# Kernel tuning notes

Hardware: AMD Instinct MI355X
Metric: run time of the kernel (lower is better)

The kernel has to match this reference:

```python
import jax, jax.numpy as jnp
import numpy as np

D = 512  # feature_dim


def _attn(q, k, v, Wq, bq, Wk, bk, Wv, bv):
    # Linear uses y = x @ W.T + b (torch convention)
    Q = jnp.einsum('bnd,od->bno', q, Wq) + bq
    K = jnp.einsum('bnd,od->bno', k, Wk) + bk
    V = jnp.einsum('bnd,od->bno', v, Wv) + bv
    scale = 1.0 / jnp.sqrt(jnp.asarray(Q.shape[-1], Q.dtype))
    scores = jnp.einsum('bqo,bko->bqk', Q, K) * scale
    attn = jax.nn.softmax(scores, axis=-1)
    return jnp.einsum('bqk,bko->bqo', attn, V)


def setup_inputs() -> dict:
    key = jax.random.key(0)
    ks = jax.random.split(key, 9)
    B, N = 8, 2048
    Itime = jax.random.normal(ks[0], (B, N, D), jnp.float32)
    Ispace = jax.random.normal(ks[1], (B, N, D), jnp.float32)
    x_origin = jax.random.normal(ks[2], (B, N, N), jnp.float32)
    # stacked params for the 4 attention blocks:
    # 0: temporal_self, 1: spatial_self, 2: temporal_guides_spatial, 3: spatial_guides_temporal
    Wq = jax.random.normal(ks[3], (4, D, D), jnp.float32) * 0.02
    Wk = jax.random.normal(ks[4], (4, D, D), jnp.float32) * 0.02
    Wv = jax.random.normal(ks[5], (4, D, D), jnp.float32) * 0.02
    bq = jax.random.normal(ks[6], (4, D), jnp.float32) * 0.02
    bk = jax.random.normal(ks[7], (4, D), jnp.float32) * 0.02
    bv = jax.random.normal(ks[8], (4, D), jnp.float32) * 0.02
    return {"Itime": Itime, "Ispace": Ispace, "x_origin": x_origin,
            "Wq": Wq, "bq": bq, "Wk": Wk, "bk": bk, "Wv": Wv, "bv": bv}


def reference(Itime, Ispace, x_origin, Wq, bq, Wk, bk, Wv, bv):
    FTT = _attn(Itime, Itime, Itime, Wq[0], bq[0], Wk[0], bk[0], Wv[0], bv[0])
    FSS = _attn(Ispace, Ispace, Ispace, Wq[1], bq[1], Wk[1], bk[1], Wv[1], bv[1])
    FTS = _attn(Itime, Ispace, Ispace, Wq[2], bq[2], Wk[2], bk[2], Wv[2], bv[2])
    FST = _attn(Ispace, Itime, Itime, Wq[3], bq[3], Wk[3], bk[3], Wv[3], bv[3])
    B, N = x_origin.shape[0], x_origin.shape[1]
    res = x_origin.reshape(B, N, -1)
    return jnp.einsum('bno,bmo->bnm', FTT + FTS, FSS + FST) + res
```

## Files before the change

### kernel.cpp

```cpp
#include <hip/hip_runtime.h>
#include <stdint.h>

typedef __bf16 bf16_t;
typedef bf16_t bf16x8 __attribute__((ext_vector_type(8)));
typedef float floatx4 __attribute__((ext_vector_type(4)));
typedef ushort ushortx8 __attribute__((ext_vector_type(8)));

__device__ __forceinline__ ushort f2bf(float f) {
  uint u = __float_as_uint(f);
  u += 0x7FFFu + ((u >> 16) & 1u);
  return (ushort)(u >> 16);
}
__device__ __forceinline__ float bf2f(ushort h) {
  return __uint_as_float(((uint)h) << 16);
}

__device__ __forceinline__ void async_cp16(const ushort* g, ushort* l) {
  __builtin_amdgcn_global_load_lds(
      (const __attribute__((address_space(1))) uint32_t*)g,
      (__attribute__((address_space(3))) uint32_t*)l, 16, 0, 0);
}

__global__ __launch_bounds__(256) void cvt_f32_bf16(const float* __restrict__ in,
                                                    ushort* __restrict__ out,
                                                    long long n) {
  long long i = (((long long)blockIdx.x) * 256 + threadIdx.x) * 4;
  if (i + 3 < n) {
    float4 f = *(const float4*)(in + i);
    ushort4 o = make_ushort4(f2bf(f.x), f2bf(f.y), f2bf(f.z), f2bf(f.w));
    *(ushort4*)(out + i) = o;
  }
}

__global__ __launch_bounds__(256) void pack_w(const float* __restrict__ Wq,
                                              const float* __restrict__ Wk,
                                              const float* __restrict__ Wv,
                                              ushort* __restrict__ Wp) {
  long long t4 = (((long long)blockIdx.x) * 256 + threadIdx.x) * 4;
  const int k = (int)(t4 & 511);
  const int jr = (int)(t4 >> 9);
  const int pi = jr / 1536;
  const int j = jr - pi * 1536;
  const int type = j >> 9;
  const int jj = j & 511;
  const float* src = (type == 0 ? Wq : type == 1 ? Wk : Wv) +
                     ((long long)(pi * 512 + jj) << 9) + k;
  float4 f = *(const float4*)src;
  ushort4 o = make_ushort4(f2bf(f.x), f2bf(f.y), f2bf(f.z), f2bf(f.w));
  *(ushort4*)(Wp + t4) = o;
}

__global__ __launch_bounds__(256) void pack_b(const float* __restrict__ bq,
                                              const float* __restrict__ bk,
                                              const float* __restrict__ bv,
                                              float* __restrict__ Bp) {
  const int i = blockIdx.x * 256 + threadIdx.x;
  const int pi = i / 1536;
  const int j = i - pi * 1536;
  const int type = j >> 9;
  const int jj = j & 511;
  Bp[i] = (type == 0 ? bq : type == 1 ? bk : bv)[pi * 512 + jj];
}

#define BM 128
#define BN 128
#define BK 64

enum { EP_QKV = 0, EP_SCALE = 2, EP_ACC = 3, EP_FINAL = 4 };

template <int MODE, bool ACCUM>
__global__ __launch_bounds__(256, 2)
void gemm_bt(const ushort* __restrict__ Aq, const ushort* __restrict__ Akv,
             const ushort* __restrict__ B,
             void* __restrict__ C, void* __restrict__ C2, void* __restrict__ C3,
             const float* __restrict__ aux,
             int M, int N, int K, int lda, int ldb, int ldc,
             long long sA, long long sB, long long sC, long long sAux,
             float scale) {
  __shared__ __align__(16) ushort sh[2][BM * BK];
  const int b = blockIdx.z;
  const int m0 = blockIdx.y * BM;
  const int n0 = blockIdx.x * BN;
  const int reg = (MODE == EP_QKV) ? (n0 >> 9) : 0;
  const ushort* Ab = ((MODE == EP_QKV && reg > 0) ? Akv : Aq) + (long long)b * sA;
  const ushort* Bb = B + (long long)b * sB;
  const int t = threadIdx.x;
  const int lane = t & 63;
  const int w = t >> 6;
  const int wr = (w >> 1) * 64;
  const int wc = (w & 1) * 64;
  const int l15 = lane & 15;
  const int quad = lane >> 4;

  floatx4 acc[4][4];
#pragma unroll
  for (int i = 0; i < 4; i++)
#pragma unroll
    for (int j = 0; j < 4; j++)
#pragma unroll
      for (int r = 0; r < 4; r++) acc[i][j][r] = 0.f;

  long long offA[4], offB[4];
  int loff[4];
#pragma unroll
  for (int i = 0; i < 4; i++) {
    const int q = w * 256 + i * 64 + lane;
    const int row = q >> 3;
    const int gk = ((q & 7) ^ (row & 7)) * 8;
    offA[i] = (long long)(m0 + row) * lda + gk;
    offB[i] = (long long)(n0 + row) * ldb + gk;
    loff[i] = (w * 256 + i * 64) * 8;
  }

  const int x7 = l15 & 7;
  for (int k0 = 0; k0 < K; k0 += BK) {
    __syncthreads();
#pragma unroll
    for (int i = 0; i < 4; i++) async_cp16(Ab + offA[i] + k0, &sh[0][loff[i]]);
#pragma unroll
    for (int i = 0; i < 4; i++) async_cp16(Bb + offB[i] + k0, &sh[1][loff[i]]);
    __syncthreads();

#pragma unroll
    for (int s = 0; s < 2; s++) {
      const int col = ((s * 4 + quad) ^ x7) * 8;
      bf16x8 af[4], bfr[4];
#pragma unroll
      for (int mi = 0; mi < 4; mi++)
        af[mi] = *(const bf16x8*)(&sh[0][0] + (wr + mi * 16 + l15) * BK + col);
#pragma unroll
      for (int ni = 0; ni < 4; ni++)
        bfr[ni] = *(const bf16x8*)(&sh[1][0] + (wc + ni * 16 + l15) * BK + col);
#pragma unroll
      for (int mi = 0; mi < 4; mi++)
#pragma unroll
        for (int ni = 0; ni < 4; ni++)
          acc[mi][ni] = __builtin_amdgcn_mfma_f32_16x16x32_bf16(
              af[mi], bfr[ni], acc[mi][ni], 0, 0, 0);
    }
  }

  float biasv[4];
  if (MODE == EP_QKV) {
#pragma unroll
    for (int ni = 0; ni < 4; ni++) biasv[ni] = aux[n0 + wc + ni * 16 + l15];
  }

  if (MODE == EP_QKV && reg == 2) {
#pragma unroll
    for (int mi = 0; mi < 4; mi++) {
#pragma unroll
      for (int ni = 0; ni < 4; ni++) {
        const int gm0 = m0 + wr + mi * 16 + quad * 4;
        const int gn = n0 + wc + ni * 16 + l15;
        const float bias = biasv[ni];
        const int b2 = gm0 >> 11;
        const int gmL = gm0 & 2047;
        ushort4 o;
        o.x = f2bf(acc[mi][ni][0] + bias);
        o.y = f2bf(acc[mi][ni][1] + bias);
        o.z = f2bf(acc[mi][ni][2] + bias);
        o.w = f2bf(acc[mi][ni][3] + bias);
        *(ushort4*)((ushort*)C2 + (long long)b2 * (512 * 2048) +
                    (long long)(gn - 1024) * 2048 + gmL) = o;
      }
    }
    return;
  }

  __syncthreads();
  float* shf = (float*)&sh[0][0];
  const int wbase = w * 1088;

#pragma unroll
  for (int mi = 0; mi < 4; mi++) {
#pragma unroll
    for (int ni = 0; ni < 4; ni++) {
#pragma unroll
      for (int r = 0; r < 4; r++) {
        float v = acc[mi][ni][r];
        if (MODE == EP_QKV) v += biasv[ni];
        if (MODE == EP_SCALE) v *= scale;
        shf[wbase + (quad * 4 + r) * 68 + ni * 16 + l15] = v;
      }
    }
    asm volatile("s_waitcnt lgkmcnt(0)" ::: "memory");
    __builtin_amdgcn_sched_barrier(0);

    const int gmb = m0 + wr + mi * 16;
    if (MODE == EP_FINAL) {
#pragma unroll
      for (int j = 0; j < 4; j++) {
        const int rr = j * 4 + (lane >> 4);
        const int c0 = (lane & 15) * 4;
        float4 f = *(const float4*)&shf[wbase + rr * 68 + c0];
        const int gm = gmb + rr;
        const int gn = n0 + wc + c0;
        float4 x = *(const float4*)(aux + (long long)b * sAux +
                                    (long long)gm * N + gn);
        f.x += x.x; f.y += x.y; f.z += x.z; f.w += x.w;
        *(float4*)((float*)C + (long long)b * sC + (long long)gm * ldc + gn) = f;
      }
    } else {
#pragma unroll
      for (int j = 0; j < 2; j++) {
        const int rr = j * 8 + (lane >> 3);
        const int c0 = (lane & 7) * 8;
        float4 f0 = *(const float4*)&shf[wbase + rr * 68 + c0];
        float4 f1 = *(const float4*)&shf[wbase + rr * 68 + c0 + 4];
        const int gm = gmb + rr;
        const int gn = n0 + wc + c0;
        float vv[8] = {f0.x, f0.y, f0.z, f0.w, f1.x, f1.y, f1.z, f1.w};
        ushort* base;
        long long off;
        if (MODE == EP_QKV) {
          if (reg == 0) { base = (ushort*)C;  off = (long long)gm * ldc + gn; }
          else          { base = (ushort*)C3; off = (long long)gm * ldc + (gn - 512); }
        } else {
          base = (ushort*)C;
          off = (long long)b * sC + (long long)gm * ldc + gn;
        }
        if (MODE == EP_ACC && ACCUM) {
          ushortx8 old = *(const ushortx8*)(base + off);
#pragma unroll
          for (int e = 0; e < 8; e++) vv[e] += bf2f(old[e]);
        }
        ushortx8 o;
#pragma unroll
        for (int e = 0; e < 8; e++) o[e] = f2bf(vv[e]);
        *(ushortx8*)(base + off) = o;
      }
    }
  }
}

__global__ __launch_bounds__(256) void softmax_rows(ushort* __restrict__ S) {
  const long long row = blockIdx.x;
  ushort* p = S + (row << 11);
  const int t = threadIdx.x;
  const int lane = t & 63;
  const int w = t >> 6;

  uint4 raw = *(const uint4*)(p + (t << 3));
  const ushort* rs = (const ushort*)&raw;
  float v[8];
  for (int i = 0; i < 8; i++) v[i] = bf2f(rs[i]);

  float mx = v[0];
  for (int i = 1; i < 8; i++) mx = fmaxf(mx, v[i]);
  for (int off = 32; off; off >>= 1) mx = fmaxf(mx, __shfl_xor(mx, off, 64));
  __shared__ float redm[4];
  __shared__ float reds[4];
  if (lane == 0) redm[w] = mx;
  __syncthreads();
  mx = fmaxf(fmaxf(redm[0], redm[1]), fmaxf(redm[2], redm[3]));

  float s = 0.f;
  for (int i = 0; i < 8; i++) {
    v[i] = __expf(v[i] - mx);
    s += v[i];
  }
  for (int off = 32; off; off >>= 1) s += __shfl_xor(s, off, 64);
  if (lane == 0) reds[w] = s;
  __syncthreads();
  s = (reds[0] + reds[1]) + (reds[2] + reds[3]);
  const float inv = 1.0f / s;

  ushort o[8];
  for (int i = 0; i < 8; i++) o[i] = f2bf(v[i] * inv);
  *(uint4*)(p + (t << 3)) = *(const uint4*)o;
}

extern "C" void kernel_launch(void* const* d_in, const int* in_sizes, int n_in,
                              void* d_out, int out_size, void* d_ws, size_t ws_size,
                              hipStream_t stream) {
  const float* Itime = (const float*)d_in[0];
  const float* Ispace = (const float*)d_in[1];
  const float* x0 = (const float*)d_in[2];
  const float* Wq = (const float*)d_in[3];
  const float* bq = (const float*)d_in[4];
  const float* Wk = (const float*)d_in[5];
  const float* bk = (const float*)d_in[6];
  const float* Wv = (const float*)d_in[7];
  const float* bv = (const float*)d_in[8];
  float* out = (float*)d_out;

  const long long SZX = 8388608;
  const long long SZWP = 4LL * 1536 * 512;
  const long long SZS = 33554432;

  ushort* p = (ushort*)d_ws;
  ushort* Tb = p;   p += SZX;
  ushort* Sb = p;   p += SZX;
  ushort* Wp = p;   p += SZWP;
  ushort* Qb = p;   p += SZX;
  ushort* Kb = p;   p += SZX;
  ushort* Vt = p;   p += SZX;
  ushort* Abf = p;  p += SZX;
  ushort* Cbf = p;  p += SZX;
  ushort* Sc = p;   p += SZS;
  float* Bp = (float*)p;

  const dim3 blk(256);
  cvt_f32_bf16<<<dim3(8192), blk, 0, stream>>>(Itime, Tb, SZX);
  cvt_f32_bf16<<<dim3(8192), blk, 0, stream>>>(Ispace, Sb, SZX);
  pack_w<<<dim3(3072), blk, 0, stream>>>(Wq, Wk, Wv, Wp);
  pack_b<<<dim3(24), blk, 0, stream>>>(bq, bk, bv, Bp);

  const float scale = 0.04419417382415922f;

  auto attn = [&](const ushort* qs, const ushort* kvs, int pi,
                  ushort* dest, bool accum) {
    const ushort* Wqi = Wp + (long long)pi * 1536 * 512;
    const float* Bqi = Bp + pi * 1536;
    gemm_bt<EP_QKV, false><<<dim3(12, 128, 1), blk, 0, stream>>>(
        qs, kvs, Wqi, Qb, Vt, Kb, Bqi, 16384, 1536, 512, 512, 512, 512,
        0, 0, 0, 0, 0.f);
    gemm_bt<EP_SCALE, false><<<dim3(16, 16, 8), blk, 0, stream>>>(
        Qb, Qb, Kb, Sc, nullptr, nullptr, nullptr, 2048, 2048, 512, 512, 512,
        2048, 1048576, 1048576, 4194304, 0, scale);
    softmax_rows<<<dim3(16384), blk, 0, stream>>>(Sc);
    if (accum)
      gemm_bt<EP_ACC, true><<<dim3(4, 16, 8), blk, 0, stream>>>(
          Sc, Sc, Vt, dest, nullptr, nullptr, nullptr, 2048, 512, 2048, 2048,
          2048, 512, 4194304, 1048576, 1048576, 0, 0.f);
    else
      gemm_bt<EP_ACC, false><<<dim3(4, 16, 8), blk, 0, stream>>>(
          Sc, Sc, Vt, dest, nullptr, nullptr, nullptr, 2048, 512, 2048, 2048,
          2048, 512, 4194304, 1048576, 1048576, 0, 0.f);
  };

  attn(Tb, Tb, 0, Abf, false);
  attn(Tb, Sb, 2, Abf, true);
  attn(Sb, Sb, 1, Cbf, false);
  attn(Sb, Tb, 3, Cbf, true);

  gemm_bt<EP_FINAL, false><<<dim3(16, 16, 8), blk, 0, stream>>>(
      Abf, Abf, Cbf, out, nullptr, nullptr, x0, 2048, 2048, 512, 512, 512,
      2048, 1048576, 1048576, 4194304, 4194304, 0.f);
}
```

Baseline: 934.3 us.

## Double-buffer GEMM LDS tiles with async prefetch and smaller K tile

The GEMM main loop now keeps two LDS buffers and prefetches the next K tile with async global-to-LDS copies while MFMAs run on the current tile. The K tile is halved to 32 so the double buffer fits in the same LDS footprint, and the swizzle is adjusted for 4 chunks per row. The aim is to hide global load latency behind compute in place of the earlier load-then-sync-then-compute sequence. The cost is one barrier per smaller K step and a different bank-conflict pattern from the new swizzle.

```diff
diff --git a/kernel.cpp b/kernel.cpp
--- a/kernel.cpp
+++ b/kernel.cpp
@@ -64,9 +64,11 @@
 
 #define BM 128
 #define BN 128
-#define BK 64
+#define BK 32
 
 enum { EP_QKV = 0, EP_SCALE = 2, EP_ACC = 3, EP_FINAL = 4 };
+
+#define SBAR0 __builtin_amdgcn_sched_barrier(0)
 
 template <int MODE, bool ACCUM>
 __global__ __launch_bounds__(256, 2)
@@ -77,7 +79,7 @@
              int M, int N, int K, int lda, int ldb, int ldc,
              long long sA, long long sB, long long sC, long long sAux,
              float scale) {
-  __shared__ __align__(16) ushort sh[2][BM * BK];
+  __shared__ __align__(16) ushort sh[2][2][BM * BK];
   const int b = blockIdx.z;
   const int m0 = blockIdx.y * BM;
   const int n0 = blockIdx.x * BN;
@@ -100,44 +102,62 @@
 #pragma unroll
       for (int r = 0; r < 4; r++) acc[i][j][r] = 0.f;
 
-  long long offA[4], offB[4];
-  int loff[4];
-#pragma unroll
-  for (int i = 0; i < 4; i++) {
-    const int q = w * 256 + i * 64 + lane;
-    const int row = q >> 3;
-    const int gk = ((q & 7) ^ (row & 7)) * 8;
+  long long offA[2], offB[2];
+  int loff[2];
+#pragma unroll
+  for (int i = 0; i < 2; i++) {
+    const int q = w * 128 + i * 64 + lane;
+    const int row = q >> 2;
+    const int c = q & 3;
+    const int gk = (c ^ ((row >> 1) & 3)) * 8;
     offA[i] = (long long)(m0 + row) * lda + gk;
     offB[i] = (long long)(n0 + row) * ldb + gk;
-    loff[i] = (w * 256 + i * 64) * 8;
-  }
-
-  const int x7 = l15 & 7;
-  for (int k0 = 0; k0 < K; k0 += BK) {
-    __syncthreads();
-#pragma unroll
-    for (int i = 0; i < 4; i++) async_cp16(Ab + offA[i] + k0, &sh[0][loff[i]]);
-#pragma unroll
-    for (int i = 0; i < 4; i++) async_cp16(Bb + offB[i] + k0, &sh[1][loff[i]]);
-    __syncthreads();
-
-#pragma unroll
-    for (int s = 0; s < 2; s++) {
-      const int col = ((s * 4 + quad) ^ x7) * 8;
-      bf16x8 af[4], bfr[4];
-#pragma unroll
-      for (int mi = 0; mi < 4; mi++)
-        af[mi] = *(const bf16x8*)(&sh[0][0] + (wr + mi * 16 + l15) * BK + col);
+    loff[i] = (w * 128 + i * 64) * 8;
+  }
+
+  const int col = ((quad ^ ((l15 >> 1) & 3)) << 3);
+  const int nt = K >> 5;
+
+#pragma unroll
+  for (int i = 0; i < 2; i++) async_cp16(Ab + offA[i], &sh[0][0][loff[i]]);
+#pragma unroll
+  for (int i = 0; i < 2; i++) async_cp16(Bb + offB[i], &sh[0][1][loff[i]]);
+  asm volatile("s_waitcnt vmcnt(0)" ::: "memory");
+  SBAR0;
+  __builtin_amdgcn_s_barrier();
+  SBAR0;
+
+  for (int kt = 0; kt < nt; ++kt) {
+    const int cur = kt & 1;
+    if (kt + 1 < nt) {
+      const int k1 = (kt + 1) << 5;
+#pragma unroll
+      for (int i = 0; i < 2; i++)
+        async_cp16(Ab + offA[i] + k1, &sh[cur ^ 1][0][loff[i]]);
+#pragma unroll
+      for (int i = 0; i < 2; i++)
+        async_cp16(Bb + offB[i] + k1, &sh[cur ^ 1][1][loff[i]]);
+    }
+    const ushort* Asb = sh[cur][0];
+    const ushort* Bsb = sh[cur][1];
+    bf16x8 af[4], bfr[4];
+#pragma unroll
+    for (int mi = 0; mi < 4; mi++)
+      af[mi] = *(const bf16x8*)(Asb + (wr + mi * 16 + l15) * BK + col);
+#pragma unroll
+    for (int ni = 0; ni < 4; ni++)
+      bfr[ni] = *(const bf16x8*)(Bsb + (wc + ni * 16 + l15) * BK + col);
+#pragma unroll
+    for (int mi = 0; mi < 4; mi++)
 #pragma unroll
       for (int ni = 0; ni < 4; ni++)
-        bfr[ni] = *(const bf16x8*)(&sh[1][0] + (wc + ni * 16 + l15) * BK + col);
-#pragma unroll
-      for (int mi = 0; mi < 4; mi++)
-#pragma unroll
-        for (int ni = 0; ni < 4; ni++)
-          acc[mi][ni] = __builtin_amdgcn_mfma_f32_16x16x32_bf16(
-              af[mi], bfr[ni], acc[mi][ni], 0, 0, 0);
-    }
+        acc[mi][ni] = __builtin_amdgcn_mfma_f32_16x16x32_bf16(
+            af[mi], bfr[ni], acc[mi][ni], 0, 0, 0);
+    SBAR0;
+    asm volatile("s_waitcnt vmcnt(0)" ::: "memory");
+    SBAR0;
+    __builtin_amdgcn_s_barrier();
+    SBAR0;
   }
 
   float biasv[4];
@@ -169,7 +189,7 @@
   }
 
   __syncthreads();
-  float* shf = (float*)&sh[0][0];
+  float* shf = (float*)&sh[0][0][0];
   const int wbase = w * 1088;
 
 #pragma unroll
```

After: 989.1 us. +5.9%, slower.

## Remap GEMM block order across XCDs and use one wave per softmax row

Applied to the files above, without the earlier changes.

The GEMM kernel now remaps its linear block index so that consecutive logical tiles are spread with stride T/8. The apparent aim is to place neighbouring tiles on the same XCD of the MI355X, which improves L2 reuse of shared A/B panels. Softmax now processes four rows per block with one wavefront per row, 32 elements per lane. This removes the shared-memory reductions and both __syncthreads barriers. The remap assumes the block count is divisible by 8 (true for all current grids) and that hardware dispatches round-robin across 8 XCDs.

```diff
diff --git a/kernel.cpp b/kernel.cpp
--- a/kernel.cpp
+++ b/kernel.cpp
@@ -78,9 +78,22 @@
              long long sA, long long sB, long long sC, long long sAux,
              float scale) {
   __shared__ __align__(16) ushort sh[2][BM * BK];
-  const int b = blockIdx.z;
-  const int m0 = blockIdx.y * BM;
-  const int n0 = blockIdx.x * BN;
+
+  int bx = blockIdx.x, by = blockIdx.y, bz = blockIdx.z;
+  {
+    const int gx = gridDim.x, gy = gridDim.y;
+    const int T = gx * gy * (int)gridDim.z;
+    int f = bx + gx * (by + gy * bz);
+    const int q = T >> 3;
+    f = (f & 7) * q + (f >> 3);
+    bx = f % gx;
+    const int r2 = f / gx;
+    by = r2 % gy;
+    bz = r2 / gy;
+  }
+  const int b = bz;
+  const int m0 = by * BM;
+  const int n0 = bx * BN;
   const int reg = (MODE == EP_QKV) ? (n0 >> 9) : 0;
   const ushort* Ab = ((MODE == EP_QKV && reg > 0) ? Akv : Aq) + (long long)b * sA;
   const ushort* Bb = B + (long long)b * sB;
@@ -235,40 +248,44 @@
 }
 
 __global__ __launch_bounds__(256) void softmax_rows(ushort* __restrict__ S) {
-  const long long row = blockIdx.x;
+  const int w = threadIdx.x >> 6;
+  const int lane = threadIdx.x & 63;
+  const long long row = (long long)blockIdx.x * 4 + w;
   ushort* p = S + (row << 11);
-  const int t = threadIdx.x;
-  const int lane = t & 63;
-  const int w = t >> 6;
-
-  uint4 raw = *(const uint4*)(p + (t << 3));
-  const ushort* rs = (const ushort*)&raw;
-  float v[8];
-  for (int i = 0; i < 8; i++) v[i] = bf2f(rs[i]);
+
+  uint4 raw[4];
+  float v[32];
+#pragma unroll
+  for (int c = 0; c < 4; c++) {
+    raw[c] = *(const uint4*)(p + (c << 9) + (lane << 3));
+    const ushort* rs = (const ushort*)&raw[c];
+#pragma unroll
+    for (int i = 0; i < 8; i++) v[c * 8 + i] = bf2f(rs[i]);
+  }
 
   float mx = v[0];
-  for (int i = 1; i < 8; i++) mx = fmaxf(mx, v[i]);
+#pragma unroll
+  for (int i = 1; i < 32; i++) mx = fmaxf(mx, v[i]);
+#pragma unroll
   for (int off = 32; off; off >>= 1) mx = fmaxf(mx, __shfl_xor(mx, off, 64));
-  __shared__ float redm[4];
-  __shared__ float reds[4];
-  if (lane == 0) redm[w] = mx;
-  __syncthreads();
-  mx = fmaxf(fmaxf(redm[0], redm[1]), fmaxf(redm[2], redm[3]));
 
   float s = 0.f;
-  for (int i = 0; i < 8; i++) {
+#pragma unroll
+  for (int i = 0; i < 32; i++) {
     v[i] = __expf(v[i] - mx);
     s += v[i];
   }
+#pragma unroll
   for (int off = 32; off; off >>= 1) s += __shfl_xor(s, off, 64);
-  if (lane == 0) reds[w] = s;
-  __syncthreads();
-  s = (reds[0] + reds[1]) + (reds[2] + reds[3]);
   const float inv = 1.0f / s;
 
-  ushort o[8];
-  for (int i = 0; i < 8; i++) o[i] = f2bf(v[i] * inv);
-  *(uint4*)(p + (t << 3)) = *(const uint4*)o;
+#pragma unroll
+  for (int c = 0; c < 4; c++) {
+    ushort o[8];
+#pragma unroll
+    for (int i = 0; i < 8; i++) o[i] = f2bf(v[c * 8 + i] * inv);
+    *(uint4*)(p + (c << 9) + (lane << 3)) = *(const uint4*)o;
+  }
 }
 
 extern "C" void kernel_launch(void* const* d_in, const int* in_sizes, int n_in,
@@ -319,7 +336,7 @@
     gemm_bt<EP_SCALE, false><<<dim3(16, 16, 8), blk, 0, stream>>>(
         Qb, Qb, Kb, Sc, nullptr, nullptr, nullptr, 2048, 2048, 512, 512, 512,
         2048, 1048576, 1048576, 4194304, 0, scale);
-    softmax_rows<<<dim3(16384), blk, 0, stream>>>(Sc);
+    softmax_rows<<<dim3(4096), blk, 0, stream>>>(Sc);
     if (accum)
       gemm_bt<EP_ACC, true><<<dim3(4, 16, 8), blk, 0, stream>>>(
           Sc, Sc, Vt, dest, nullptr, nullptr, nullptr, 2048, 512, 2048, 2048,
```

New measurement: 805.2 us. -13.8%, faster.
